# Optimization experiments

Measured on AMD Instinct MI355X. Metric: run time of the kernel, lower is better.

## Reference

```python
import jax, jax.numpy as jnp
import numpy as np
from jax import lax

K = 16
SIGMA2 = 1.0  # sigma=1.0 squared
EPS = 1e-06


def setup_inputs() -> dict:
    key = jax.random.key(0)
    xyz = jax.random.normal(key, (4, 3, 4096), dtype=jnp.float32)
    return {"xyz": xyz}


def reference(xyz):
    # xyz: (B, 3, N)
    B, _, N = xyz.shape
    pts = jnp.transpose(xyz, (0, 2, 1))  # (B, N, 3)

    sq = jnp.sum(pts * pts, axis=-1)  # (B, N)
    d2 = sq[:, :, None] + sq[:, None, :] - 2.0 * jnp.einsum("bnd,bmd->bnm", pts, pts)

    # k nearest neighbors (smallest distance, includes self like torch knn on same set)
    _, idx = lax.top_k(-d2, K)  # idx: (B, N, K)

    # gather neighbor coordinates and recompute exact squared distance (faithful to source)
    neighbors = jax.vmap(lambda p, i: p[i])(pts, idx)  # (B, N, K, 3)
    diff = pts[:, :, None, :] - neighbors
    dist2 = jnp.sum(diff * diff, axis=-1)  # (B, N, K)
    weights = jnp.exp(-dist2 / (2.0 * SIGMA2))

    # scatter k-sparse weights into dense adjacency (topk indices per row are unique)
    bb = jnp.arange(B)[:, None, None]
    ii = jnp.arange(N)[None, :, None]
    A = jnp.zeros((B, N, N), dtype=xyz.dtype).at[bb, ii, idx].set(weights)
    A = 0.5 * (A + jnp.swapaxes(A, 1, 2))

    # symmetric normalized Laplacian L = I - D^{-1/2} A D^{-1/2} (diag scaling via broadcast)
    D = jnp.clip(jnp.sum(A, axis=-1), EPS, None)
    d_is = D ** -0.5  # (B, N)
    L = jnp.eye(N, dtype=xyz.dtype)[None] - d_is[:, :, None] * A * d_is[:, None, :]
    return L
```

## Files before the change

### kernel.cpp

```cpp
#include <hip/hip_runtime.h>
#include <math.h>

#pragma clang fp contract(off)

#define NPTS 4096
#define KNN  16
#define RPBK 32
#define KT   1024
#define CAP  128
#define CAPIN 64
#define SPILLCAP 262144
#define RROWS 4

typedef float nfloat4 __attribute__((ext_vector_type(4)));

__device__ __forceinline__ unsigned okey(float f) {
    f = f + 0.0f;
    unsigned u = __float_as_uint(f);
    return u ^ (((unsigned)((int)u >> 31)) | 0x80000000u);
}

__device__ __forceinline__ unsigned long long wmin64(unsigned long long v) {
    for (int o = 32; o > 0; o >>= 1) { unsigned long long w = __shfl_xor(v, o); v = w < v ? w : v; }
    return v;
}

__device__ __forceinline__ float disv(const float* __restrict__ Dsum, int i) {
    return 1.0f / sqrtf(fmaxf(Dsum[i], 1e-6f));
}

__global__ void zero_kernel(float* __restrict__ p, int n) {
    int i = blockIdx.x * blockDim.x + threadIdx.x;
    if (i < n) p[i] = 0.0f;
}

__device__ __forceinline__ float thresh16(float k, int lane) {
    int rank = 0;
#pragma unroll
    for (int s = 0; s < 64; ++s) {
        float ks = __shfl(k, s);
        rank += (ks < k || (ks == k && s < lane)) ? 1 : 0;
    }
    unsigned long long m = __ballot(rank == 15);
    return __shfl(k, __ffsll(m) - 1);
}

__device__ __forceinline__ int select16(const float* __restrict__ sx,
                                        const float* __restrict__ sy,
                                        const float* __restrict__ sz,
                                        const int* __restrict__ list,
                                        int cnt2, float4 P, int lane) {
    if (cnt2 <= 64) {
        float key = __builtin_huge_valf();
        int m = -1;
        if (lane < cnt2) {
            m = list[lane];
            float qx = sx[m], qy = sy[m], qz = sz[m];
            float qw = (qx * qx + qy * qy) + qz * qz;
            float dot = (P.x * qx + P.y * qy) + P.z * qz;
            key = (P.w + qw) - 2.0f * dot;
        }
        int rank = 0;
#pragma unroll
        for (int s = 0; s < 64; ++s) {
            float ks = __shfl(key, s);
            rank += (ks < key || (ks == key && s < lane)) ? 1 : 0;
        }
        return __builtin_amdgcn_ds_permute(rank << 2, m);
    }
    if (cnt2 <= CAP) {
        unsigned long long e0 = ~0ull, e1 = ~0ull;
        if (lane < cnt2) {
            int m = list[lane];
            float qx = sx[m], qy = sy[m], qz = sz[m];
            float qw = (qx * qx + qy * qy) + qz * qz;
            float dot = (P.x * qx + P.y * qy) + P.z * qz;
            float d2  = (P.w + qw) - 2.0f * dot;
            e0 = ((unsigned long long)okey(d2) << 32) | (unsigned)m;
        }
        if (lane + 64 < cnt2) {
            int m = list[lane + 64];
            float qx = sx[m], qy = sy[m], qz = sz[m];
            float qw = (qx * qx + qy * qy) + qz * qz;
            float dot = (P.x * qx + P.y * qy) + P.z * qz;
            float d2  = (P.w + qw) - 2.0f * dot;
            e1 = ((unsigned long long)okey(d2) << 32) | (unsigned)m;
        }
        int selm = -1;
        unsigned long long c = e0 < e1 ? e0 : e1;
        for (int r = 0; r < KNN; ++r) {
            unsigned long long mn = wmin64(c);
            if (c == mn) {
                if (e0 == mn) e0 = ~0ull; else e1 = ~0ull;
                c = e0 < e1 ? e0 : e1;
            }
            if (lane == r) selm = (int)(unsigned)(mn & 0xFFFFFFFFull);
        }
        return selm;
    }
    unsigned long long last = 0; int selm = -1;
    for (int r = 0; r < KNN; ++r) {
        unsigned long long bestp = ~0ull;
        for (int i = 0; i < NPTS / 64; ++i) {
            int m = i * 64 + lane;
            float qx = sx[m], qy = sy[m], qz = sz[m];
            float qw = (qx * qx + qy * qy) + qz * qz;
            float dot = (P.x * qx + P.y * qy) + P.z * qz;
            float d2  = (P.w + qw) - 2.0f * dot;
            unsigned long long key = ((unsigned long long)okey(d2) << 32) | (unsigned)m;
            if (key > last && key < bestp) bestp = key;
        }
        unsigned long long mn = wmin64(bestp);
        if (lane == r) selm = (int)(unsigned)(mn & 0xFFFFFFFFull);
        last = mn;
    }
    return selm;
}

__device__ __forceinline__ void emit_row(int rowg, int b, int selm, float4 P,
                                         const float* __restrict__ sx,
                                         const float* __restrict__ sy,
                                         const float* __restrict__ sz,
                                         float* __restrict__ Dsum,
                                         int* __restrict__ idx_out,
                                         float* __restrict__ w_out,
                                         int* __restrict__ cnt,
                                         int* __restrict__ inc,
                                         int* __restrict__ spillc,
                                         int* __restrict__ spill,
                                         int do_inc, int lane) {
    float wgt = 0.0f;
    if (lane < KNN) {
        int j = selm;
        float dx = P.x - sx[j], dy = P.y - sy[j], dz = P.z - sz[j];
        float dist2 = (dx * dx + dy * dy) + dz * dz;
        wgt = expf(-(dist2 * 0.5f));
        size_t base = (size_t)rowg * KNN + lane;
        idx_out[base] = j;
        w_out[base]   = wgt;
        int jg = (b << 12) + j;
        atomicAdd(&Dsum[jg], 0.5f * wgt);
        if (do_inc) {
            int pos = atomicAdd(&cnt[jg], 1);
            if (pos < CAPIN) {
                inc[(size_t)jg * CAPIN + pos] = (int)base;
            } else {
                int sp = atomicAdd(spillc, 1);
                if (sp < SPILLCAP) spill[sp] = (int)base;
            }
        }
    }
    float rs = wgt;
    for (int o = 32; o > 0; o >>= 1) rs += __shfl_xor(rs, o);
    if (lane == 0) atomicAdd(&Dsum[rowg], 0.5f * rs);
}

__global__ __launch_bounds__(KT, 8) void knn_kernel(const float* __restrict__ xyz,
                                                    float* __restrict__ Dsum,
                                                    int* __restrict__ idx_out,
                                                    float* __restrict__ w_out,
                                                    int* __restrict__ cnt,
                                                    int* __restrict__ inc,
                                                    int* __restrict__ spillc,
                                                    int* __restrict__ spill,
                                                    int do_inc) {
    __shared__ float sx[NPTS], sy[NPTS], sz[NPTS];
    __shared__ int   lists[RPBK][CAP];

    const int t    = threadIdx.x;
    const int lane = t & 63;
    const int wv   = t >> 6;
    const int row0 = blockIdx.x * RPBK + 2 * wv;
    const int b    = row0 >> 12;
    const float* X = xyz + (size_t)b * 3 * NPTS;

    for (int i = t; i < NPTS; i += KT) {
        sx[i] = X[i]; sy[i] = X[NPTS + i]; sz[i] = X[2 * NPTS + i];
    }
    __syncthreads();

    const int ra = row0 & (NPTS - 1), rb = (row0 + 1) & (NPTS - 1);
    float4 PA, PB;
    PA.x = sx[ra]; PA.y = sy[ra]; PA.z = sz[ra];
    PA.w = (PA.x * PA.x + PA.y * PA.y) + PA.z * PA.z;
    PB.x = sx[rb]; PB.y = sy[rb]; PB.z = sz[rb];
    PB.w = (PB.x * PB.x + PB.y * PB.y) + PB.z * PB.z;

    float bA = __builtin_huge_valf(), bB = __builtin_huge_valf();
    for (int i = 0; i < NPTS / 64; ++i) {
        int m = i * 64 + lane;
        float qx = sx[m], qy = sy[m], qz = sz[m];
        float qw = (qx * qx + qy * qy) + qz * qz;
        float dotA = (PA.x * qx + PA.y * qy) + PA.z * qz;
        float d2A  = (PA.w + qw) - 2.0f * dotA;
        float dotB = (PB.x * qx + PB.y * qy) + PB.z * qz;
        float d2B  = (PB.w + qw) - 2.0f * dotB;
        bA = fminf(bA, d2A);
        bB = fminf(bB, d2B);
    }
    const float TA = thresh16(bA, lane);
    const float TB = thresh16(bB, lane);

    int* listA = &lists[2 * wv][0];
    int* listB = &lists[2 * wv + 1][0];
    int cA = 0, cB = 0;
    for (int i = 0; i < NPTS / 64; ++i) {
        int m = i * 64 + lane;
        float qx = sx[m], qy = sy[m], qz = sz[m];
        float qw = (qx * qx + qy * qy) + qz * qz;
        float dotA = (PA.x * qx + PA.y * qy) + PA.z * qz;
        float d2A  = (PA.w + qw) - 2.0f * dotA;
        float dotB = (PB.x * qx + PB.y * qy) + PB.z * qz;
        float d2B  = (PB.w + qw) - 2.0f * dotB;
        bool pA = d2A <= TA;
        unsigned long long balA = __ballot(pA);
        if (pA) {
            int pos = cA + __popcll(balA & ((1ull << lane) - 1ull));
            if (pos < CAP) listA[pos] = m;
        }
        cA += (int)__popcll(balA);
        bool pB = d2B <= TB;
        unsigned long long balB = __ballot(pB);
        if (pB) {
            int pos = cB + __popcll(balB & ((1ull << lane) - 1ull));
            if (pos < CAP) listB[pos] = m;
        }
        cB += (int)__popcll(balB);
    }

    int selA = select16(sx, sy, sz, listA, cA, PA, lane);
    int selB = select16(sx, sy, sz, listB, cB, PB, lane);
    emit_row(row0,     b, selA, PA, sx, sy, sz, Dsum, idx_out, w_out,
             cnt, inc, spillc, spill, do_inc, lane);
    emit_row(row0 + 1, b, selB, PB, sx, sy, sz, Dsum, idx_out, w_out,
             cnt, inc, spillc, spill, do_inc, lane);
}

__global__ __launch_bounds__(1024, 4) void row_kernel(const int* __restrict__ idxb,
                                                      const float* __restrict__ wb,
                                                      const float* __restrict__ Dsum,
                                                      const int* __restrict__ cnt,
                                                      const int* __restrict__ inc,
                                                      const int* __restrict__ spillc,
                                                      const int* __restrict__ spill,
                                                      float* __restrict__ L) {
    __shared__ float row[RROWS * NPTS];
    const int r0 = blockIdx.x * RROWS;
    const int b  = r0 >> 12;

    float4* row4 = (float4*)row;
    for (int i = threadIdx.x; i < RROWS * NPTS / 4; i += 1024)
        row4[i] = make_float4(0.0f, 0.0f, 0.0f, 0.0f);
    __syncthreads();

    const int rr = threadIdx.x >> 8;
    const int tt = threadIdx.x & 255;
    const int r  = r0 + rr;
    float* myrow = row + rr * NPTS;
    const float dn = disv(Dsum, r);

    if (tt < KNN) {
        int g = r * KNN + tt;
        int j = idxb[g];
        float v = -0.5f * wb[g] * dn * disv(Dsum, (b << 12) + j);
        atomicAdd(&myrow[j], v);
    }
    int c = cnt[r];
    if (c > CAPIN) c = CAPIN;
    for (int i = tt; i < c; i += 256) {
        int g   = inc[(size_t)r * CAPIN + i];
        int src = g >> 4;
        float v = -0.5f * wb[g] * disv(Dsum, src) * dn;
        atomicAdd(&myrow[src & (NPTS - 1)], v);
    }

    int sc = spillc[0];
    if (sc > 0) {
        if (sc > SPILLCAP) sc = SPILLCAP;
        for (int i = threadIdx.x; i < sc; i += 1024) {
            int g   = spill[i];
            int src = g >> 4;
            int jg  = ((src >> 12) << 12) + idxb[g];
            if (jg >= r0 && jg < r0 + RROWS) {
                float v = -0.5f * wb[g] * disv(Dsum, src) * disv(Dsum, jg);
                atomicAdd(&row[(jg - r0) * NPTS + (src & (NPTS - 1))], v);
            }
        }
    }
    __syncthreads();

    const int n0 = r0 & (NPTS - 1);
    nfloat4* Lr = (nfloat4*)(L + (size_t)b * NPTS * NPTS + (size_t)n0 * NPTS);
    const nfloat4* row4n = (const nfloat4*)row;
    for (int q = threadIdx.x; q < RROWS * NPTS / 4; q += 1024) {
        nfloat4 v = row4n[q];
        int n = n0 + (q >> 10);
        if ((q & 1023) == (n >> 2)) v[n & 3] += 1.0f;
        __builtin_nontemporal_store(v, &Lr[q]);
    }
}

__global__ void dis_kernel(const float* __restrict__ Dsum, float* __restrict__ dis, int n) {
    int i = blockIdx.x * blockDim.x + threadIdx.x;
    if (i < n) dis[i] = 1.0f / sqrtf(fmaxf(Dsum[i], 1e-6f));
}

__global__ __launch_bounds__(256) void fill_kernel(float4* __restrict__ L4, size_t T4) {
    size_t g4     = (size_t)blockIdx.x * blockDim.x + threadIdx.x;
    size_t stride = (size_t)gridDim.x * blockDim.x;
    for (; g4 < T4; g4 += stride) {
        size_t g = g4 << 2;
        int o    = (int)(g & (size_t)(NPTS * (size_t)NPTS - 1));
        int row  = o >> 12;
        int col0 = o & (NPTS - 1);
        float4 v;
        v.x = (row == col0    ) ? 1.0f : 0.0f;
        v.y = (row == col0 + 1) ? 1.0f : 0.0f;
        v.z = (row == col0 + 2) ? 1.0f : 0.0f;
        v.w = (row == col0 + 3) ? 1.0f : 0.0f;
        L4[g4] = v;
    }
}

__global__ __launch_bounds__(256) void scatter_kernel(const int* __restrict__ idxb,
                                                      const float* __restrict__ wb,
                                                      const float* __restrict__ dis,
                                                      float* __restrict__ L) {
    int g   = blockIdx.x * 256 + threadIdx.x;
    int row = g >> 4;
    int b   = row >> 12;
    int n   = row & (NPTS - 1);
    int j   = idxb[g];
    float v = -0.5f * wb[g] * dis[row] * dis[(b << 12) + j];
    float* Lb = L + (size_t)b * NPTS * NPTS;
    atomicAdd(Lb + (size_t)n * NPTS + j, v);
    atomicAdd(Lb + (size_t)j * NPTS + n, v);
}

extern "C" void kernel_launch(void* const* d_in, const int* in_sizes, int n_in,
                              void* d_out, int out_size, void* d_ws, size_t ws_size,
                              hipStream_t stream) {
    const float* xyz = (const float*)d_in[0];
    const int B  = in_sizes[0] / (3 * NPTS);
    const int BN = B * NPTS;

    float* Dsum   = (float*)d_ws;
    int*   cnt    = (int*)(Dsum + BN);
    int*   spillc = cnt + BN;
    int*   idxb   = (int*)(spillc + 16);
    float* wb     = (float*)(idxb + (size_t)BN * KNN);
    int*   inc    = (int*)(wb + (size_t)BN * KNN);
    int*   spill  = inc + (size_t)BN * CAPIN;
    float* L      = (float*)d_out;

    size_t need = ((size_t)BN * (2 + 2 * KNN + CAPIN) + 16 + SPILLCAP) * 4;
    const int fused = (ws_size >= need);

    if (fused) {
        int nz = 2 * BN + 16;
        zero_kernel<<<(nz + 255) / 256, 256, 0, stream>>>(Dsum, nz);
        knn_kernel<<<BN / RPBK, KT, 0, stream>>>(xyz, Dsum, idxb, wb,
                                                 cnt, inc, spillc, spill, 1);
        row_kernel<<<BN / RROWS, 1024, 0, stream>>>(idxb, wb, Dsum,
                                                    cnt, inc, spillc, spill, L);
    } else {
        float* fDsum = (float*)d_ws;
        float* fdis  = fDsum + BN;
        int*   fidx  = (int*)(fdis + BN);
        float* fwb   = (float*)(fidx + (size_t)BN * KNN);
        zero_kernel<<<BN / 256, 256, 0, stream>>>(fDsum, BN);
        knn_kernel<<<BN / RPBK, KT, 0, stream>>>(xyz, fDsum, fidx, fwb,
                                                 nullptr, nullptr, nullptr, nullptr, 0);
        dis_kernel<<<BN / 256, 256, 0, stream>>>(fDsum, fdis, BN);
        size_t T4 = (size_t)B * NPTS * NPTS / 4;
        fill_kernel<<<8192, 256, 0, stream>>>((float4*)d_out, T4);
        scatter_kernel<<<(BN * KNN) / 256, 256, 0, stream>>>(fidx, fwb, fdis, L);
    }
}
```

Measured before the change: 363.3 us.

## Process four rows per wavefront in KNN and use FMA distance filtering

Each wavefront now handles four query rows instead of two, so every shared-memory load of candidate coordinates serves more distance computations. The distance math uses fused multiply-adds, and each threshold gets a small margin so rounding differences do not drop true neighbours. The 65-128 candidate selection path is removed and the list capacity shrinks to 64, so larger lists fall back to the slow full-scan path. The risks are higher register pressure and more frequent fallbacks caused by the widened threshold.

```diff
diff --git a/kernel.cpp b/kernel.cpp
--- a/kernel.cpp
+++ b/kernel.cpp
@@ -5,9 +5,10 @@
 
 #define NPTS 4096
 #define KNN  16
-#define RPBK 32
+#define RW   4
+#define RPBK 64
 #define KT   1024
-#define CAP  128
+#define CAP  64
 #define CAPIN 64
 #define SPILLCAP 262144
 #define RROWS 4
@@ -67,36 +68,6 @@
             rank += (ks < key || (ks == key && s < lane)) ? 1 : 0;
         }
         return __builtin_amdgcn_ds_permute(rank << 2, m);
-    }
-    if (cnt2 <= CAP) {
-        unsigned long long e0 = ~0ull, e1 = ~0ull;
-        if (lane < cnt2) {
-            int m = list[lane];
-            float qx = sx[m], qy = sy[m], qz = sz[m];
-            float qw = (qx * qx + qy * qy) + qz * qz;
-            float dot = (P.x * qx + P.y * qy) + P.z * qz;
-            float d2  = (P.w + qw) - 2.0f * dot;
-            e0 = ((unsigned long long)okey(d2) << 32) | (unsigned)m;
-        }
-        if (lane + 64 < cnt2) {
-            int m = list[lane + 64];
-            float qx = sx[m], qy = sy[m], qz = sz[m];
-            float qw = (qx * qx + qy * qy) + qz * qz;
-            float dot = (P.x * qx + P.y * qy) + P.z * qz;
-            float d2  = (P.w + qw) - 2.0f * dot;
-            e1 = ((unsigned long long)okey(d2) << 32) | (unsigned)m;
-        }
-        int selm = -1;
-        unsigned long long c = e0 < e1 ? e0 : e1;
-        for (int r = 0; r < KNN; ++r) {
-            unsigned long long mn = wmin64(c);
-            if (c == mn) {
-                if (e0 == mn) e0 = ~0ull; else e1 = ~0ull;
-                c = e0 < e1 ? e0 : e1;
-            }
-            if (lane == r) selm = (int)(unsigned)(mn & 0xFFFFFFFFull);
-        }
-        return selm;
     }
     unsigned long long last = 0; int selm = -1;
     for (int r = 0; r < KNN; ++r) {
@@ -170,7 +141,7 @@
     const int t    = threadIdx.x;
     const int lane = t & 63;
     const int wv   = t >> 6;
-    const int row0 = blockIdx.x * RPBK + 2 * wv;
+    const int row0 = blockIdx.x * RPBK + wv * RW;
     const int b    = row0 >> 12;
     const float* X = xyz + (size_t)b * 3 * NPTS;
 
@@ -179,61 +150,67 @@
     }
     __syncthreads();
 
-    const int ra = row0 & (NPTS - 1), rb = (row0 + 1) & (NPTS - 1);
-    float4 PA, PB;
-    PA.x = sx[ra]; PA.y = sy[ra]; PA.z = sz[ra];
-    PA.w = (PA.x * PA.x + PA.y * PA.y) + PA.z * PA.z;
-    PB.x = sx[rb]; PB.y = sy[rb]; PB.z = sz[rb];
-    PB.w = (PB.x * PB.x + PB.y * PB.y) + PB.z * PB.z;
-
-    float bA = __builtin_huge_valf(), bB = __builtin_huge_valf();
+    float Px[RW], Py[RW], Pz[RW], Pw[RW];
+#pragma unroll
+    for (int r = 0; r < RW; ++r) {
+        int rr = (row0 + r) & (NPTS - 1);
+        Px[r] = sx[rr]; Py[r] = sy[rr]; Pz[r] = sz[rr];
+        Pw[r] = (Px[r] * Px[r] + Py[r] * Py[r]) + Pz[r] * Pz[r];
+    }
+
+    float bm[RW];
+#pragma unroll
+    for (int r = 0; r < RW; ++r) bm[r] = __builtin_huge_valf();
     for (int i = 0; i < NPTS / 64; ++i) {
         int m = i * 64 + lane;
         float qx = sx[m], qy = sy[m], qz = sz[m];
-        float qw = (qx * qx + qy * qy) + qz * qz;
-        float dotA = (PA.x * qx + PA.y * qy) + PA.z * qz;
-        float d2A  = (PA.w + qw) - 2.0f * dotA;
-        float dotB = (PB.x * qx + PB.y * qy) + PB.z * qz;
-        float d2B  = (PB.w + qw) - 2.0f * dotB;
-        bA = fminf(bA, d2A);
-        bB = fminf(bB, d2B);
-    }
-    const float TA = thresh16(bA, lane);
-    const float TB = thresh16(bB, lane);
-
-    int* listA = &lists[2 * wv][0];
-    int* listB = &lists[2 * wv + 1][0];
-    int cA = 0, cB = 0;
+        float qwF = __builtin_fmaf(qz, qz, __builtin_fmaf(qy, qy, qx * qx));
+#pragma unroll
+        for (int r = 0; r < RW; ++r) {
+            float dot = __builtin_fmaf(qz, Pz[r],
+                         __builtin_fmaf(qy, Py[r], qx * Px[r]));
+            float d2  = __builtin_fmaf(-2.0f, dot, Pw[r] + qwF);
+            bm[r] = fminf(bm[r], d2);
+        }
+    }
+    float T[RW];
+#pragma unroll
+    for (int r = 0; r < RW; ++r) {
+        float tt = thresh16(bm[r], lane);
+        T[r] = tt + (fabsf(tt) * 4e-6f + 1e-4f);
+    }
+
+    int cc[RW];
+#pragma unroll
+    for (int r = 0; r < RW; ++r) cc[r] = 0;
     for (int i = 0; i < NPTS / 64; ++i) {
         int m = i * 64 + lane;
         float qx = sx[m], qy = sy[m], qz = sz[m];
-        float qw = (qx * qx + qy * qy) + qz * qz;
-        float dotA = (PA.x * qx + PA.y * qy) + PA.z * qz;
-        float d2A  = (PA.w + qw) - 2.0f * dotA;
-        float dotB = (PB.x * qx + PB.y * qy) + PB.z * qz;
-        float d2B  = (PB.w + qw) - 2.0f * dotB;
-        bool pA = d2A <= TA;
-        unsigned long long balA = __ballot(pA);
-        if (pA) {
-            int pos = cA + __popcll(balA & ((1ull << lane) - 1ull));
-            if (pos < CAP) listA[pos] = m;
-        }
-        cA += (int)__popcll(balA);
-        bool pB = d2B <= TB;
-        unsigned long long balB = __ballot(pB);
-        if (pB) {
-            int pos = cB + __popcll(balB & ((1ull << lane) - 1ull));
-            if (pos < CAP) listB[pos] = m;
-        }
-        cB += (int)__popcll(balB);
-    }
-
-    int selA = select16(sx, sy, sz, listA, cA, PA, lane);
-    int selB = select16(sx, sy, sz, listB, cB, PB, lane);
-    emit_row(row0,     b, selA, PA, sx, sy, sz, Dsum, idx_out, w_out,
-             cnt, inc, spillc, spill, do_inc, lane);
-    emit_row(row0 + 1, b, selB, PB, sx, sy, sz, Dsum, idx_out, w_out,
-             cnt, inc, spillc, spill, do_inc, lane);
+        float qwF = __builtin_fmaf(qz, qz, __builtin_fmaf(qy, qy, qx * qx));
+#pragma unroll
+        for (int r = 0; r < RW; ++r) {
+            float dot = __builtin_fmaf(qz, Pz[r],
+                         __builtin_fmaf(qy, Py[r], qx * Px[r]));
+            float d2  = __builtin_fmaf(-2.0f, dot, Pw[r] + qwF);
+            bool pass = d2 <= T[r];
+            unsigned long long bal = __ballot(pass);
+            if (bal) {
+                if (pass) {
+                    int pos = cc[r] + __popcll(bal & ((1ull << lane) - 1ull));
+                    if (pos < CAP) lists[wv * RW + r][pos] = m;
+                }
+                cc[r] += (int)__popcll(bal);
+            }
+        }
+    }
+
+#pragma unroll
+    for (int r = 0; r < RW; ++r) {
+        float4 P = make_float4(Px[r], Py[r], Pz[r], Pw[r]);
+        int sel = select16(sx, sy, sz, &lists[wv * RW + r][0], cc[r], P, lane);
+        emit_row(row0 + r, b, sel, P, sx, sy, sz, Dsum, idx_out, w_out,
+                 cnt, inc, spillc, spill, do_inc, lane);
+    }
 }
 
 __global__ __launch_bounds__(1024, 4) void row_kernel(const int* __restrict__ idxb,
```

Result: faster. 342.8 us (-5.7%).
